# Kernel optimization log

Measured on AMD Instinct MI355X. Metric: run time of the kernel, lower is better.

The kernel has to match this reference:

```python
import jax, jax.numpy as jnp
import numpy as np

NUM_SCENES = 7
SHAPE = [512, 512, 256, 64]  # layer dims: 512->512->256->64
BATCH = 16384


def _xavier(key, shape):
    # nn.init.xavier_normal_ on (s, in, out): fan_in/fan_out from last two dims
    fan_in, fan_out = shape[-2], shape[-1]
    std = np.sqrt(2.0 / (fan_in + fan_out)).astype(np.float32)
    return jax.random.normal(key, shape, dtype=jnp.float32) * std


def setup_inputs() -> dict:
    key = jax.random.key(0)
    ks = jax.random.split(key, 16)
    inp = {
        "x": jax.random.normal(ks[0], (BATCH, SHAPE[0]), dtype=jnp.float32),
        "scene": jax.random.randint(ks[1], (BATCH,), 1, NUM_SCENES + 1, dtype=jnp.int64),
    }
    for i in range(3):
        din, dout = SHAPE[i], SHAPE[i + 1]
        inp[f"W{i}"] = _xavier(ks[2 + 4 * i], (NUM_SCENES, din, dout))
        inp[f"b{i}"] = jnp.zeros((NUM_SCENES, dout), dtype=jnp.float32)
        inp[f"gW{i}"] = _xavier(ks[3 + 4 * i], (1, din, dout))
        inp[f"gb{i}"] = jnp.zeros((1, dout), dtype=jnp.float32)
    return inp


def _star_linear(x, scene0, W, b, gW, gb, relu):
    # W: (S, in, out), gW: (1, in, out). Equivalent to gathering W[scene0]
    # and doing x[:,None,:] @ (w * gW), but computed as a dense GEMM over
    # all scenes followed by a per-sample select (avoids B*in*out gather).
    scaled = W * gW                                   # (S, in, out)
    out_all = jnp.einsum('bi,sio->bso', x, scaled)    # (B, S, out)
    out = jnp.take_along_axis(out_all, scene0[:, None, None], axis=1)[:, 0, :]
    out = out + b[scene0] + gb[0]
    if relu:
        out = jnp.maximum(out, 0.0)
    return out  # dropout is identity at eval


def reference(x, scene, W0, b0, gW0, gb0, W1, b1, gW1, gb1, W2, b2, gW2, gb2):
    scene0 = (scene - 1).astype(jnp.int32)
    h = _star_linear(x, scene0, W0, b0, gW0, gb0, relu=True)
    h = _star_linear(h, scene0, W1, b1, gW1, gb1, relu=True)
    h = _star_linear(h, scene0, W2, b2, gW2, gb2, relu=False)  # drop=True -> no relu
    return h
```

## Files before the change

kernel.cpp:

```cpp
#include <hip/hip_runtime.h>
#include <hip/hip_bf16.h>
#include <stdint.h>


#define BATCH   16384
#define NSCENE  7
#define TM      128
#define NBLK    (BATCH / 256)
#define MT_MAX  (BATCH / TM + NSCENE)
#define PADMAX  (BATCH + NSCENE * TM)

typedef __bf16 bf16x8 __attribute__((ext_vector_type(8)));
typedef float  f32x4  __attribute__((ext_vector_type(4)));

__device__ __forceinline__ ushort f2bf(float f) {
  union { float f; uint32_t u; } v; v.f = f;
  uint32_t r = (v.u + 0x7FFFu + ((v.u >> 16) & 1u)) >> 16;
  return (ushort)r;
}
__device__ __forceinline__ uint32_t pk2(float a, float b) {
  union { __hip_bfloat162 h; uint32_t u; } cv;
  cv.h = __float22bfloat162_rn(make_float2(a, b));
  return cv.u;
}
__device__ __forceinline__ void async16(const void* g, void* lds) {
  __builtin_amdgcn_global_load_lds(
      (const __attribute__((address_space(1))) uint32_t*)g,
      (__attribute__((address_space(3))) uint32_t*)lds, 16, 0, 0);
}

__device__ __forceinline__ void st_tile(const float* __restrict__ W,
                                        const float* __restrict__ gW,
                                        ushort* __restrict__ sT,
                                        int K, int N, int s, int n0, int k0,
                                        int tid) {
  __shared__ float tl[32][33];
  int tx = tid & 31, ty = tid >> 5;
  const float* Wp = W + (size_t)s * K * N;
#pragma unroll
  for (int i = 0; i < 4; i++) {
    int k = k0 + ty + i * 8;
    tl[ty + i * 8][tx] = Wp[(size_t)k * N + n0 + tx] * gW[(size_t)k * N + n0 + tx];
  }
  __syncthreads();
#pragma unroll
  for (int i = 0; i < 4; i++) {
    int n = n0 + ty + i * 8;
    sT[((size_t)s * N + n) * K + k0 + tx] = f2bf(tl[tx][ty + i * 8]);
  }
}

#define NB_W0 (16 * 16 * 7)
#define NB_W1 (8 * 16 * 7)
#define NB_W2 (2 * 8 * 7)
#define NB_BIAS 23
#define NB_CNT NBLK

__global__ __launch_bounds__(256) void prep_k(
    const float* __restrict__ W0, const float* __restrict__ gW0,
    const float* __restrict__ W1, const float* __restrict__ gW1,
    const float* __restrict__ W2, const float* __restrict__ gW2,
    const float* __restrict__ b0, const float* __restrict__ gb0,
    const float* __restrict__ b1, const float* __restrict__ gb1,
    const float* __restrict__ b2, const float* __restrict__ gb2,
    const int* __restrict__ scene,
    ushort* __restrict__ sT0, ushort* __restrict__ sT1, ushort* __restrict__ sT2,
    float* __restrict__ bias0, float* __restrict__ bias1, float* __restrict__ bias2,
    int* __restrict__ bcnt) {
  int bid = blockIdx.x, tid = threadIdx.x;
  if (bid < NB_W0) {
    int l = bid;
    st_tile(W0, gW0, sT0, 512, 512, l / 256, (l % 16) * 32, ((l / 16) % 16) * 32, tid);
  } else if (bid < NB_W0 + NB_W1) {
    int l = bid - NB_W0;
    st_tile(W1, gW1, sT1, 512, 256, l / 128, (l % 8) * 32, ((l / 8) % 16) * 32, tid);
  } else if (bid < NB_W0 + NB_W1 + NB_W2) {
    int l = bid - NB_W0 - NB_W1;
    st_tile(W2, gW2, sT2, 256, 64, l / 16, (l % 2) * 32, ((l / 2) % 8) * 32, tid);
  } else if (bid < NB_W0 + NB_W1 + NB_W2 + NB_BIAS) {
    int t = (bid - NB_W0 - NB_W1 - NB_W2) * 256 + tid;
    if (t < 7 * 512) bias0[t] = b0[t] + gb0[t & 511];
    else if (t < 7 * 512 + 7 * 256) { int i = t - 7 * 512; bias1[i] = b1[i] + gb1[i & 255]; }
    else if (t < 7 * 512 + 7 * 256 + 7 * 64) { int i = t - 7 * 512 - 7 * 256; bias2[i] = b2[i] + gb2[i & 63]; }
  } else {
    __shared__ int l[NSCENE];
    if (tid < NSCENE) l[tid] = 0;
    __syncthreads();
    int blk = bid - NB_W0 - NB_W1 - NB_W2 - NB_BIAS;
    atomicAdd(&l[scene[blk * 256 + tid] - 1], 1);
    __syncthreads();
    if (tid < NSCENE) bcnt[blk * NSCENE + tid] = l[tid];
  }
}

__global__ void plan_k(const int* __restrict__ bcnt, int* __restrict__ meta,
                       int* __restrict__ bbase, int* __restrict__ idxp) {
  __shared__ int tot[NSCENE], pstart[NSCENE], pend[NSCENE];
  int tid = threadIdx.x;
  if (tid < NSCENE) {
    int c = 0;
    for (int b = 0; b < NBLK; b++) c += bcnt[b * NSCENE + tid];
    tot[tid] = c;
  }
  __syncthreads();
  if (tid == 0) {
    int po = 0, t = 0;
    for (int s = 0; s < NSCENE; s++) {
      meta[16 + s] = po;
      int tiles = (tot[s] + TM - 1) / TM;
      pstart[s] = po + tot[s];
      pend[s] = po + tiles * TM;
      for (int j = 0; j < tiles; j++) { meta[32 + t] = s; meta[192 + t] = po + j * TM; t++; }
      po += tiles * TM;
    }
    meta[24] = t;
  }
  __syncthreads();
  if (tid < NSCENE) {
    int run = meta[16 + tid];
    for (int b = 0; b < NBLK; b++) { bbase[b * NSCENE + tid] = run; run += bcnt[b * NSCENE + tid]; }
  }
  for (int s = 0; s < NSCENE; s++)
    for (int i = pstart[s] + tid; i < pend[s]; i += 256) idxp[i] = -1;
}

__global__ __launch_bounds__(256) void scatxc_k(const int* __restrict__ scene,
                                                const int* __restrict__ bbase,
                                                const float* __restrict__ x,
                                                int* __restrict__ idxp,
                                                ushort* __restrict__ xc) {
  __shared__ int l[NSCENE];
  __shared__ int sdest[256];
  int tid = threadIdx.x, bid = blockIdx.x;
  if (tid < NSCENE) l[tid] = 0;
  __syncthreads();
  int i = bid * 256 + tid;
  int s = scene[i] - 1;
  int pos = atomicAdd(&l[s], 1);
  int dest = bbase[bid * NSCENE + s] + pos;
  idxp[dest] = i;
  sdest[tid] = dest;
  __syncthreads();
  int rbase = bid * 256;
#pragma unroll 4
  for (int p = 0; p < 32; p++) {
    int rl = p * 8 + (tid >> 5);
    int c = (tid & 31) * 16;
    int d = sdest[rl];
    const float4* pp = (const float4*)(x + (size_t)(rbase + rl) * 512 + c);
    float4 f0 = pp[0], f1 = pp[1], f2 = pp[2], f3 = pp[3];
    uint4 v0, v1;
    v0.x = pk2(f0.x, f0.y); v0.y = pk2(f0.z, f0.w);
    v0.z = pk2(f1.x, f1.y); v0.w = pk2(f1.z, f1.w);
    v1.x = pk2(f2.x, f2.y); v1.y = pk2(f2.z, f2.w);
    v1.z = pk2(f3.x, f3.y); v1.w = pk2(f3.z, f3.w);
    uint4* q = (uint4*)(xc + (size_t)d * 512 + c);
    q[0] = v0; q[1] = v1;
  }
}

__global__ __launch_bounds__(256) void gemm0_k(
    const ushort* __restrict__ ain, const ushort* __restrict__ bw,
    const float* __restrict__ bias, const int* __restrict__ meta,
    ushort* __restrict__ hout) {
  int t = blockIdx.x;
  if (t >= meta[24]) return;
  int sc = meta[32 + t];
  int mrow0 = meta[192 + t];
  int nb = blockIdx.y;

  __shared__ __align__(16) ushort Abuf[TM * 64];
  __shared__ __align__(16) ushort Bbuf[TM * 64];

  int tid = threadIdx.x;
  int lane = tid & 63, wid = tid >> 6;
  int wm = wid >> 1, wn = wid & 1;

  f32x4 acc[4][4];
#pragma unroll
  for (int mt = 0; mt < 4; mt++)
#pragma unroll
    for (int nt = 0; nt < 4; nt++) acc[mt][nt] = (f32x4){0.f, 0.f, 0.f, 0.f};

  const ushort* bwS = bw + ((size_t)sc * 512 + (size_t)nb * 128) * 512;

  for (int kb = 0; kb < 8; kb++) {
#pragma unroll
    for (int i = 0; i < 4; i++) {
      int c = tid + i * 256;
      int row = c >> 3, q = c & 7;
      int kg = q ^ (row & 7);
      async16(ain + (size_t)(mrow0 + row) * 512 + kb * 64 + kg * 8,
              &Abuf[(size_t)(i * 256 + wid * 64) * 8]);
    }
#pragma unroll
    for (int i = 0; i < 4; i++) {
      int c = tid + i * 256;
      int row = c >> 3, q = c & 7;
      int kg = q ^ (row & 7);
      async16(bwS + (size_t)row * 512 + kb * 64 + kg * 8,
              &Bbuf[(size_t)(i * 256 + wid * 64) * 8]);
    }
    __syncthreads();
#pragma unroll
    for (int kk = 0; kk < 64; kk += 32) {
      bf16x8 af[4], bfr[4];
      int kc = (kk >> 3) + (lane >> 4);
#pragma unroll
      for (int mt = 0; mt < 4; mt++) {
        int row = wm * 64 + mt * 16 + (lane & 15);
        af[mt] = *(const bf16x8*)(&Abuf[(row * 8 + (kc ^ (row & 7))) * 8]);
      }
#pragma unroll
      for (int nt = 0; nt < 4; nt++) {
        int row = wn * 64 + nt * 16 + (lane & 15);
        bfr[nt] = *(const bf16x8*)(&Bbuf[(row * 8 + (kc ^ (row & 7))) * 8]);
      }
#pragma unroll
      for (int mt = 0; mt < 4; mt++)
#pragma unroll
        for (int nt = 0; nt < 4; nt++)
          acc[mt][nt] = __builtin_amdgcn_mfma_f32_16x16x32_bf16(af[mt], bfr[nt], acc[mt][nt], 0, 0, 0);
    }
    __syncthreads();
  }

#pragma unroll
  for (int mt = 0; mt < 4; mt++) {
    int rl0 = wm * 64 + mt * 16 + (lane >> 4) * 4;
#pragma unroll
    for (int nt = 0; nt < 4; nt++) {
      int col = nb * 128 + wn * 64 + nt * 16 + (lane & 15);
      float bv = bias[sc * 512 + col];
#pragma unroll
      for (int r = 0; r < 4; r++) {
        float v = fmaxf(acc[mt][nt][r] + bv, 0.f);
        hout[(size_t)(mrow0 + rl0 + r) * 512 + col] = f2bf(v);
      }
    }
  }
}

__global__ __launch_bounds__(512) void gemm12_k(
    const ushort* __restrict__ hc1, const ushort* __restrict__ sT1,
    const ushort* __restrict__ sT2, const float* __restrict__ bias1,
    const float* __restrict__ bias2, const int* __restrict__ meta,
    const int* __restrict__ idxp, float* __restrict__ out) {
  int t = blockIdx.x;
  if (t >= meta[24]) return;
  int sc = meta[32 + t];
  int mrow0 = meta[192 + t];

  __shared__ __align__(16) ushort Abuf[128 * 64];
  __shared__ __align__(16) ushort Bbuf[256 * 64];
  __shared__ __align__(16) ushort h2[128 * 256];

  int tid = threadIdx.x;
  int lane = tid & 63, wid = tid >> 6;
  int wm = wid >> 2, wn = wid & 3;

  f32x4 acc[4][4];
#pragma unroll
  for (int mt = 0; mt < 4; mt++)
#pragma unroll
    for (int nt = 0; nt < 4; nt++) acc[mt][nt] = (f32x4){0.f, 0.f, 0.f, 0.f};

  const ushort* b1p = sT1 + (size_t)sc * 256 * 512;

  for (int kb = 0; kb < 8; kb++) {
#pragma unroll
    for (int i = 0; i < 2; i++) {
      int c = tid + i * 512;
      int row = c >> 3, q = c & 7;
      int kg = q ^ (row & 7);
      async16(hc1 + (size_t)(mrow0 + row) * 512 + kb * 64 + kg * 8,
              &Abuf[(size_t)(i * 512 + wid * 64) * 8]);
    }
#pragma unroll
    for (int i = 0; i < 4; i++) {
      int c = tid + i * 512;
      int row = c >> 3, q = c & 7;
      int kg = q ^ (row & 7);
      async16(b1p + (size_t)row * 512 + kb * 64 + kg * 8,
              &Bbuf[(size_t)(i * 512 + wid * 64) * 8]);
    }
    __syncthreads();
#pragma unroll
    for (int kk = 0; kk < 64; kk += 32) {
      bf16x8 af[4], bfr[4];
      int kc = (kk >> 3) + (lane >> 4);
#pragma unroll
      for (int mt = 0; mt < 4; mt++) {
        int row = wm * 64 + mt * 16 + (lane & 15);
        af[mt] = *(const bf16x8*)(&Abuf[(row * 8 + (kc ^ (row & 7))) * 8]);
      }
#pragma unroll
      for (int nt = 0; nt < 4; nt++) {
        int row = wn * 64 + nt * 16 + (lane & 15);
        bfr[nt] = *(const bf16x8*)(&Bbuf[(row * 8 + (kc ^ (row & 7))) * 8]);
      }
#pragma unroll
      for (int mt = 0; mt < 4; mt++)
#pragma unroll
        for (int nt = 0; nt < 4; nt++)
          acc[mt][nt] = __builtin_amdgcn_mfma_f32_16x16x32_bf16(af[mt], bfr[nt], acc[mt][nt], 0, 0, 0);
    }
    __syncthreads();
  }

#pragma unroll
  for (int mt = 0; mt < 4; mt++) {
#pragma unroll
    for (int nt = 0; nt < 4; nt++) {
      int col = wn * 64 + nt * 16 + (lane & 15);
      float bv = bias1[sc * 256 + col];
#pragma unroll
      for (int r = 0; r < 4; r++) {
        int row = wm * 64 + mt * 16 + (lane >> 4) * 4 + r;
        float v = fmaxf(acc[mt][nt][r] + bv, 0.f);
        h2[(row * 32 + ((col >> 3) ^ (row & 7))) * 8 + (col & 7)] = f2bf(v);
      }
    }
  }
  __syncthreads();

  f32x4 acc2[4];
#pragma unroll
  for (int mt = 0; mt < 4; mt++) acc2[mt] = (f32x4){0.f, 0.f, 0.f, 0.f};

  const ushort* b2p = sT2 + (size_t)sc * 64 * 256;

  for (int kb = 0; kb < 4; kb++) {
    {
      int c = tid;
      int row = c >> 3, q = c & 7;
      int kg = q ^ (row & 7);
      async16(b2p + (size_t)row * 256 + kb * 64 + kg * 8,
              &Bbuf[(size_t)(wid * 64) * 8]);
    }
    __syncthreads();
#pragma unroll
    for (int kk = 0; kk < 64; kk += 32) {
      bf16x8 af[4], bfr;
      int kc = (kk >> 3) + (lane >> 4);
      int kf = kb * 8 + kc;
#pragma unroll
      for (int mt = 0; mt < 4; mt++) {
        int row = wm * 64 + mt * 16 + (lane & 15);
        af[mt] = *(const bf16x8*)(&h2[(row * 32 + (kf ^ (row & 7))) * 8]);
      }
      {
        int n = wn * 16 + (lane & 15);
        bfr = *(const bf16x8*)(&Bbuf[(n * 8 + (kc ^ (n & 7))) * 8]);
      }
#pragma unroll
      for (int mt = 0; mt < 4; mt++)
        acc2[mt] = __builtin_amdgcn_mfma_f32_16x16x32_bf16(af[mt], bfr, acc2[mt], 0, 0, 0);
    }
    __syncthreads();
  }

  int col = wn * 16 + (lane & 15);
  float bv = bias2[sc * 64 + col];
#pragma unroll
  for (int mt = 0; mt < 4; mt++) {
    int rl0 = wm * 64 + mt * 16 + (lane >> 4) * 4;
#pragma unroll
    for (int r = 0; r < 4; r++) {
      int g = idxp[mrow0 + rl0 + r];
      if (g >= 0) out[(size_t)g * 64 + col] = acc2[mt][r] + bv;
    }
  }
}

extern "C" void kernel_launch(void* const* d_in, const int* in_sizes, int n_in,
                              void* d_out, int out_size, void* d_ws, size_t ws_size,
                              hipStream_t stream) {
  const float* x   = (const float*)d_in[0];
  const int* scene = (const int*)d_in[1];
  const float* W0  = (const float*)d_in[2];
  const float* b0  = (const float*)d_in[3];
  const float* gW0 = (const float*)d_in[4];
  const float* gb0 = (const float*)d_in[5];
  const float* W1  = (const float*)d_in[6];
  const float* b1  = (const float*)d_in[7];
  const float* gW1 = (const float*)d_in[8];
  const float* gb1 = (const float*)d_in[9];
  const float* W2  = (const float*)d_in[10];
  const float* b2  = (const float*)d_in[11];
  const float* gW2 = (const float*)d_in[12];
  const float* gb2 = (const float*)d_in[13];
  float* out = (float*)d_out;

  char* ws = (char*)d_ws;
  size_t off = 0;
  auto alloc = [&](size_t bytes) -> void* {
    void* p = ws + off;
    off = (off + bytes + 255) & ~(size_t)255;
    return p;
  };
  ushort* sT0   = (ushort*)alloc((size_t)7 * 512 * 512 * 2);
  ushort* sT1   = (ushort*)alloc((size_t)7 * 256 * 512 * 2);
  ushort* sT2   = (ushort*)alloc((size_t)7 * 64 * 256 * 2);
  float*  bias0 = (float*)alloc(7 * 512 * 4);
  float*  bias1 = (float*)alloc(7 * 256 * 4);
  float*  bias2 = (float*)alloc(7 * 64 * 4);
  int*    meta  = (int*)alloc(1024 * 4);
  int*    bcnt  = (int*)alloc(NBLK * NSCENE * 4);
  int*    bbase = (int*)alloc(NBLK * NSCENE * 4);
  int*    idxp  = (int*)alloc(PADMAX * 4);
  ushort* xc    = (ushort*)alloc((size_t)PADMAX * 512 * 2);
  ushort* hc1   = (ushort*)alloc((size_t)PADMAX * 512 * 2);
  (void)ws_size; (void)n_in; (void)in_sizes; (void)out_size;

  prep_k<<<NB_W0 + NB_W1 + NB_W2 + NB_BIAS + NB_CNT, 256, 0, stream>>>(
      W0, gW0, W1, gW1, W2, gW2, b0, gb0, b1, gb1, b2, gb2, scene,
      sT0, sT1, sT2, bias0, bias1, bias2, bcnt);
  plan_k<<<1, 256, 0, stream>>>(bcnt, meta, bbase, idxp);
  scatxc_k<<<NBLK, 256, 0, stream>>>(scene, bbase, x, idxp, xc);

  gemm0_k<<<dim3(MT_MAX, 4), 256, 0, stream>>>(xc, sT0, bias0, meta, hc1);
  gemm12_k<<<dim3(MT_MAX), 512, 0, stream>>>(hc1, sT1, sT2, bias1, bias2,
                                             meta, idxp, out);
}
```

Baseline: 187.0 us.

## Split gather/convert into many small blocks and halve gemm12 row tiles

The per-block rank of each sample within its scene is now computed in the prep kernel and stored, so the x gather/bf16-convert kernel needs no shared-memory atomics and runs as 2048 small blocks of 8 rows each instead of 64 large blocks. The fused layer-1/layer-2 kernel now uses 64-row tiles with 256 threads, doubling the grid. It also loads the whole layer-2 weight tile once, overlapped with the h2 write, which removes the per-k-block barriers in the second GEMM. The intent is more parallelism on a 256-CU GPU and less synchronisation, at the cost of reloading layer-1 weights twice as often and one extra rank buffer.

```diff
diff --git a/kernel.cpp b/kernel.cpp
--- a/kernel.cpp
+++ b/kernel.cpp
@@ -66,7 +66,7 @@
     const int* __restrict__ scene,
     ushort* __restrict__ sT0, ushort* __restrict__ sT1, ushort* __restrict__ sT2,
     float* __restrict__ bias0, float* __restrict__ bias1, float* __restrict__ bias2,
-    int* __restrict__ bcnt) {
+    int* __restrict__ bcnt, int* __restrict__ rank) {
   int bid = blockIdx.x, tid = threadIdx.x;
   if (bid < NB_W0) {
     int l = bid;
@@ -87,7 +87,9 @@
     if (tid < NSCENE) l[tid] = 0;
     __syncthreads();
     int blk = bid - NB_W0 - NB_W1 - NB_W2 - NB_BIAS;
-    atomicAdd(&l[scene[blk * 256 + tid] - 1], 1);
+    int i = blk * 256 + tid;
+    int pos = atomicAdd(&l[scene[i] - 1], 1);
+    rank[i] = pos;
     __syncthreads();
     if (tid < NSCENE) bcnt[blk * NSCENE + tid] = l[tid];
   }
@@ -124,39 +126,26 @@
     for (int i = pstart[s] + tid; i < pend[s]; i += 256) idxp[i] = -1;
 }
 
-__global__ __launch_bounds__(256) void scatxc_k(const int* __restrict__ scene,
-                                                const int* __restrict__ bbase,
-                                                const float* __restrict__ x,
-                                                int* __restrict__ idxp,
-                                                ushort* __restrict__ xc) {
-  __shared__ int l[NSCENE];
-  __shared__ int sdest[256];
-  int tid = threadIdx.x, bid = blockIdx.x;
-  if (tid < NSCENE) l[tid] = 0;
-  __syncthreads();
-  int i = bid * 256 + tid;
-  int s = scene[i] - 1;
-  int pos = atomicAdd(&l[s], 1);
-  int dest = bbase[bid * NSCENE + s] + pos;
-  idxp[dest] = i;
-  sdest[tid] = dest;
-  __syncthreads();
-  int rbase = bid * 256;
-#pragma unroll 4
-  for (int p = 0; p < 32; p++) {
-    int rl = p * 8 + (tid >> 5);
-    int c = (tid & 31) * 16;
-    int d = sdest[rl];
-    const float4* pp = (const float4*)(x + (size_t)(rbase + rl) * 512 + c);
-    float4 f0 = pp[0], f1 = pp[1], f2 = pp[2], f3 = pp[3];
-    uint4 v0, v1;
-    v0.x = pk2(f0.x, f0.y); v0.y = pk2(f0.z, f0.w);
-    v0.z = pk2(f1.x, f1.y); v0.w = pk2(f1.z, f1.w);
-    v1.x = pk2(f2.x, f2.y); v1.y = pk2(f2.z, f2.w);
-    v1.z = pk2(f3.x, f3.y); v1.w = pk2(f3.z, f3.w);
-    uint4* q = (uint4*)(xc + (size_t)d * 512 + c);
-    q[0] = v0; q[1] = v1;
-  }
+__global__ __launch_bounds__(256) void xc_k(const float* __restrict__ x,
+                                            const int* __restrict__ scene,
+                                            const int* __restrict__ rank,
+                                            const int* __restrict__ bbase,
+                                            int* __restrict__ idxp,
+                                            ushort* __restrict__ xc) {
+  int r = blockIdx.x * 8 + (threadIdx.x >> 5);
+  int s = scene[r] - 1;
+  int d = bbase[(r >> 8) * NSCENE + s] + rank[r];
+  if ((threadIdx.x & 31) == 0) idxp[d] = r;
+  int c = (threadIdx.x & 31) * 16;
+  const float4* p = (const float4*)(x + (size_t)r * 512 + c);
+  float4 f0 = p[0], f1 = p[1], f2 = p[2], f3 = p[3];
+  uint4 v0, v1;
+  v0.x = pk2(f0.x, f0.y); v0.y = pk2(f0.z, f0.w);
+  v0.z = pk2(f1.x, f1.y); v0.w = pk2(f1.z, f1.w);
+  v1.x = pk2(f2.x, f2.y); v1.y = pk2(f2.z, f2.w);
+  v1.z = pk2(f3.x, f3.y); v1.w = pk2(f3.z, f3.w);
+  uint4* q = (uint4*)(xc + (size_t)d * 512 + c);
+  q[0] = v0; q[1] = v1;
 }
 
 __global__ __launch_bounds__(256) void gemm0_k(
@@ -241,23 +230,23 @@
   }
 }
 
-__global__ __launch_bounds__(512) void gemm12_k(
+__global__ __launch_bounds__(256) void gemm12_k(
     const ushort* __restrict__ hc1, const ushort* __restrict__ sT1,
     const ushort* __restrict__ sT2, const float* __restrict__ bias1,
     const float* __restrict__ bias2, const int* __restrict__ meta,
     const int* __restrict__ idxp, float* __restrict__ out) {
-  int t = blockIdx.x;
+  int j = blockIdx.x;
+  int t = j >> 1;
   if (t >= meta[24]) return;
   int sc = meta[32 + t];
-  int mrow0 = meta[192 + t];
-
-  __shared__ __align__(16) ushort Abuf[128 * 64];
+  int mrow0 = meta[192 + t] + (j & 1) * 64;
+
+  __shared__ __align__(16) ushort Abuf[64 * 64];
   __shared__ __align__(16) ushort Bbuf[256 * 64];
-  __shared__ __align__(16) ushort h2[128 * 256];
+  __shared__ __align__(16) ushort h2[64 * 256];
 
   int tid = threadIdx.x;
   int lane = tid & 63, wid = tid >> 6;
-  int wm = wid >> 2, wn = wid & 3;
 
   f32x4 acc[4][4];
 #pragma unroll
@@ -270,19 +259,19 @@
   for (int kb = 0; kb < 8; kb++) {
 #pragma unroll
     for (int i = 0; i < 2; i++) {
-      int c = tid + i * 512;
+      int c = tid + i * 256;
       int row = c >> 3, q = c & 7;
       int kg = q ^ (row & 7);
       async16(hc1 + (size_t)(mrow0 + row) * 512 + kb * 64 + kg * 8,
-              &Abuf[(size_t)(i * 512 + wid * 64) * 8]);
-    }
-#pragma unroll
-    for (int i = 0; i < 4; i++) {
-      int c = tid + i * 512;
+              &Abuf[(size_t)(i * 256 + wid * 64) * 8]);
+    }
+#pragma unroll
+    for (int i = 0; i < 8; i++) {
+      int c = tid + i * 256;
       int row = c >> 3, q = c & 7;
       int kg = q ^ (row & 7);
       async16(b1p + (size_t)row * 512 + kb * 64 + kg * 8,
-              &Bbuf[(size_t)(i * 512 + wid * 64) * 8]);
+              &Bbuf[(size_t)(i * 256 + wid * 64) * 8]);
     }
     __syncthreads();
 #pragma unroll
@@ -291,12 +280,12 @@
       int kc = (kk >> 3) + (lane >> 4);
 #pragma unroll
       for (int mt = 0; mt < 4; mt++) {
-        int row = wm * 64 + mt * 16 + (lane & 15);
+        int row = mt * 16 + (lane & 15);
         af[mt] = *(const bf16x8*)(&Abuf[(row * 8 + (kc ^ (row & 7))) * 8]);
       }
 #pragma unroll
       for (int nt = 0; nt < 4; nt++) {
-        int row = wn * 64 + nt * 16 + (lane & 15);
+        int row = wid * 64 + nt * 16 + (lane & 15);
         bfr[nt] = *(const bf16x8*)(&Bbuf[(row * 8 + (kc ^ (row & 7))) * 8]);
       }
 #pragma unroll
@@ -312,63 +301,63 @@
   for (int mt = 0; mt < 4; mt++) {
 #pragma unroll
     for (int nt = 0; nt < 4; nt++) {
-      int col = wn * 64 + nt * 16 + (lane & 15);
+      int col = wid * 64 + nt * 16 + (lane & 15);
       float bv = bias1[sc * 256 + col];
 #pragma unroll
       for (int r = 0; r < 4; r++) {
-        int row = wm * 64 + mt * 16 + (lane >> 4) * 4 + r;
+        int row = mt * 16 + (lane >> 4) * 4 + r;
         float v = fmaxf(acc[mt][nt][r] + bv, 0.f);
         h2[(row * 32 + ((col >> 3) ^ (row & 7))) * 8 + (col & 7)] = f2bf(v);
       }
     }
   }
+
+  const ushort* b2p = sT2 + (size_t)sc * 64 * 256;
+#pragma unroll
+  for (int i = 0; i < 8; i++) {
+    int p = tid + i * 256;
+    int row = p >> 5, pc = p & 31;
+    int kg = pc ^ (row & 7);
+    async16(b2p + (size_t)row * 256 + kg * 8,
+            &Bbuf[(size_t)(i * 256 + wid * 64) * 8]);
+  }
   __syncthreads();
 
   f32x4 acc2[4];
 #pragma unroll
-  for (int mt = 0; mt < 4; mt++) acc2[mt] = (f32x4){0.f, 0.f, 0.f, 0.f};
-
-  const ushort* b2p = sT2 + (size_t)sc * 64 * 256;
-
-  for (int kb = 0; kb < 4; kb++) {
+  for (int nt = 0; nt < 4; nt++) acc2[nt] = (f32x4){0.f, 0.f, 0.f, 0.f};
+
+#pragma unroll
+  for (int kk = 0; kk < 256; kk += 32) {
+    int kf = (kk >> 3) + (lane >> 4);
+    bf16x8 af;
     {
-      int c = tid;
-      int row = c >> 3, q = c & 7;
-      int kg = q ^ (row & 7);
-      async16(b2p + (size_t)row * 256 + kb * 64 + kg * 8,
-              &Bbuf[(size_t)(wid * 64) * 8]);
-    }
-    __syncthreads();
-#pragma unroll
-    for (int kk = 0; kk < 64; kk += 32) {
-      bf16x8 af[4], bfr;
-      int kc = (kk >> 3) + (lane >> 4);
-      int kf = kb * 8 + kc;
-#pragma unroll
-      for (int mt = 0; mt < 4; mt++) {
-        int row = wm * 64 + mt * 16 + (lane & 15);
-        af[mt] = *(const bf16x8*)(&h2[(row * 32 + (kf ^ (row & 7))) * 8]);
-      }
-      {
-        int n = wn * 16 + (lane & 15);
-        bfr = *(const bf16x8*)(&Bbuf[(n * 8 + (kc ^ (n & 7))) * 8]);
-      }
-#pragma unroll
-      for (int mt = 0; mt < 4; mt++)
-        acc2[mt] = __builtin_amdgcn_mfma_f32_16x16x32_bf16(af[mt], bfr, acc2[mt], 0, 0, 0);
-    }
-    __syncthreads();
-  }
-
-  int col = wn * 16 + (lane & 15);
-  float bv = bias2[sc * 64 + col];
-#pragma unroll
-  for (int mt = 0; mt < 4; mt++) {
-    int rl0 = wm * 64 + mt * 16 + (lane >> 4) * 4;
+      int row = wid * 16 + (lane & 15);
+      af = *(const bf16x8*)(&h2[(row * 32 + (kf ^ (row & 7))) * 8]);
+    }
+    bf16x8 bfr[4];
+#pragma unroll
+    for (int nt = 0; nt < 4; nt++) {
+      int n = nt * 16 + (lane & 15);
+      bfr[nt] = *(const bf16x8*)(&Bbuf[(n * 32 + (kf ^ (n & 7))) * 8]);
+    }
+#pragma unroll
+    for (int nt = 0; nt < 4; nt++)
+      acc2[nt] = __builtin_amdgcn_mfma_f32_16x16x32_bf16(af, bfr[nt], acc2[nt], 0, 0, 0);
+  }
+
+  int gidx[4];
+#pragma unroll
+  for (int r = 0; r < 4; r++)
+    gidx[r] = idxp[mrow0 + wid * 16 + (lane >> 4) * 4 + r];
+#pragma unroll
+  for (int nt = 0; nt < 4; nt++) {
+    int col = nt * 16 + (lane & 15);
+    float bv = bias2[sc * 64 + col];
 #pragma unroll
     for (int r = 0; r < 4; r++) {
-      int g = idxp[mrow0 + rl0 + r];
-      if (g >= 0) out[(size_t)g * 64 + col] = acc2[mt][r] + bv;
+      int g = gidx[r];
+      if (g >= 0) out[(size_t)g * 64 + col] = acc2[nt][r] + bv;
     }
   }
 }
@@ -408,6 +397,7 @@
   int*    meta  = (int*)alloc(1024 * 4);
   int*    bcnt  = (int*)alloc(NBLK * NSCENE * 4);
   int*    bbase = (int*)alloc(NBLK * NSCENE * 4);
+  int*    rank  = (int*)alloc(BATCH * 4);
   int*    idxp  = (int*)alloc(PADMAX * 4);
   ushort* xc    = (ushort*)alloc((size_t)PADMAX * 512 * 2);
   ushort* hc1   = (ushort*)alloc((size_t)PADMAX * 512 * 2);
@@ -415,11 +405,11 @@
 
   prep_k<<<NB_W0 + NB_W1 + NB_W2 + NB_BIAS + NB_CNT, 256, 0, stream>>>(
       W0, gW0, W1, gW1, W2, gW2, b0, gb0, b1, gb1, b2, gb2, scene,
-      sT0, sT1, sT2, bias0, bias1, bias2, bcnt);
+      sT0, sT1, sT2, bias0, bias1, bias2, bcnt, rank);
   plan_k<<<1, 256, 0, stream>>>(bcnt, meta, bbase, idxp);
-  scatxc_k<<<NBLK, 256, 0, stream>>>(scene, bbase, x, idxp, xc);
+  xc_k<<<BATCH / 8, 256, 0, stream>>>(x, scene, rank, bbase, idxp, xc);
 
   gemm0_k<<<dim3(MT_MAX, 4), 256, 0, stream>>>(xc, sT0, bias0, meta, hc1);
-  gemm12_k<<<dim3(MT_MAX), 512, 0, stream>>>(hc1, sT1, sT2, bias1, bias2,
-                                             meta, idxp, out);
-}
+  gemm12_k<<<dim3(MT_MAX * 2), 256, 0, stream>>>(hc1, sT1, sT2, bias1, bias2,
+                                                 meta, idxp, out);
+}
```

After: 164.6 us. 1.14x faster.
